# Optimization experiments

Hardware: AMD Instinct MI355X
Metric: run time of the kernel (lower is better)

Reference implementation:

```python
import jax, jax.numpy as jnp
import numpy as np

S, B, D, H = 2048, 2, 1024, 16
DK = D // H
SCALE = 1.0 / np.sqrt(DK)


def setup_inputs() -> dict:
    key = jax.random.key(0)
    ks = jax.random.split(key, 8)
    return {
        "query": jax.random.normal(ks[0], (S, B, D), dtype=jnp.float32),
        "key": jax.random.normal(ks[1], (S, B, D), dtype=jnp.float32),
        "value": jax.random.normal(ks[2], (S, B, D), dtype=jnp.float32),
        "mask": jax.random.randint(ks[3], (B, S, S), 0, 2, dtype=jnp.int32),
        "in_proj_weight": jax.random.normal(ks[4], (3 * D, D), dtype=jnp.float32) * 0.02,
        "in_proj_bias": jax.random.normal(ks[5], (3 * D,), dtype=jnp.float32) * 0.02,
        "out_proj_weight": jax.random.normal(ks[6], (D, D), dtype=jnp.float32) * 0.02,
        "out_proj_bias": jax.random.normal(ks[7], (D,), dtype=jnp.float32) * 0.02,
    }


def reference(query, key, value, mask, in_proj_weight, in_proj_bias,
              out_proj_weight, out_proj_bias):
    seq_len, batch, d_model = query.shape
    # split fused in-projection: order is query, key, value
    Wq, Wk, Wv = in_proj_weight[:D], in_proj_weight[D:2 * D], in_proj_weight[2 * D:]
    bq, bk, bv = in_proj_bias[:D], in_proj_bias[D:2 * D], in_proj_bias[2 * D:]
    # PrepareForMultiHeadAttention: x @ W^T + b, then split heads -> [s, b, h, d_k]
    q = (query @ Wq.T + bq).reshape(seq_len, batch, H, DK)
    k = (key @ Wk.T + bk).reshape(key.shape[0], batch, H, DK)
    v = (value @ Wv.T + bv).reshape(value.shape[0], batch, H, DK)
    # scores [i, j, b, h] in float32, scaled
    scores = jnp.einsum('ibhd,jbhd->ijbh', q, k).astype(jnp.float32) * SCALE
    # mask: [b, q, k] -> permute(1,2,0) -> [q, k, b] -> unsqueeze(-1)
    m = jnp.transpose(mask, (1, 2, 0))[..., None]
    scores = jnp.where(m == 1, jnp.float32(-1e9), scores)
    # softmax over key axis (dim=1)
    attn = jax.nn.softmax(scores, axis=1)
    # dropout p=0.0 -> identity
    x = jnp.einsum('ijbh,jbhd->ibhd', attn, v).reshape(seq_len, batch, -1)
    return x @ out_proj_weight.T + out_proj_bias
```

## Files before the change

kernel.cpp:

```cpp
#include <hip/hip_runtime.h>
#include <hip/hip_bf16.h>

typedef unsigned short u16;
typedef unsigned int   u32;
typedef unsigned long long u64;
typedef __bf16 bf16x8 __attribute__((ext_vector_type(8)));
typedef float  f32x4  __attribute__((ext_vector_type(4)));

#define S_LEN  2048
#define BATCH  2
#define DMODEL 1024
#define NHEADS 16
#define DKH    64
#define MWORDS (S_LEN/64)
#define ATT_SCALE 0.125f
#define C2EXP 0.18033688011112f

__device__ __forceinline__ u16 f2bf(float f){
  u32 x = __builtin_bit_cast(u32, f);
  x += 0x7fffu + ((x >> 16) & 1u);
  return (u16)(x >> 16);
}
__device__ __forceinline__ bf16x8 ld8(const u16* p){ return *(const bf16x8*)p; }

__device__ __forceinline__ void gload16(const u16* g, u16* l){
  __builtin_amdgcn_global_load_lds(
      (const __attribute__((address_space(1))) u32*)(u64)g,
      (__attribute__((address_space(3))) u32*)(u64)l,
      16, 0, 0);
}

__global__ __launch_bounds__(256) void cvt_kernel(
    const float* __restrict__ a0, const float* __restrict__ a1, const float* __restrict__ a2,
    const float* __restrict__ wi, const float* __restrict__ wo, const int* __restrict__ msk,
    u16* __restrict__ d0, u16* __restrict__ d1, u16* __restrict__ d2,
    u16* __restrict__ dwi, u16* __restrict__ dwo, u64* __restrict__ mbits)
{
  int tid = blockIdx.x*256 + threadIdx.x;
  int stride = gridDim.x*256;
  const int NX = S_LEN*BATCH*DMODEL/4;
  for (int i = tid; i < NX; i += stride){
    f32x4 x0 = ((const f32x4*)a0)[i];
    f32x4 x1 = ((const f32x4*)a1)[i];
    f32x4 x2 = ((const f32x4*)a2)[i];
    ((ushort4*)d0)[i] = make_ushort4(f2bf(x0[0]), f2bf(x0[1]), f2bf(x0[2]), f2bf(x0[3]));
    ((ushort4*)d1)[i] = make_ushort4(f2bf(x1[0]), f2bf(x1[1]), f2bf(x1[2]), f2bf(x1[3]));
    ((ushort4*)d2)[i] = make_ushort4(f2bf(x2[0]), f2bf(x2[1]), f2bf(x2[2]), f2bf(x2[3]));
  }
  const int NWI = 3*DMODEL*DMODEL/4;
  for (int i = tid; i < NWI; i += stride){
    f32x4 x = ((const f32x4*)wi)[i];
    ((ushort4*)dwi)[i] = make_ushort4(f2bf(x[0]), f2bf(x[1]), f2bf(x[2]), f2bf(x[3]));
  }
  const int NWO = DMODEL*DMODEL/4;
  for (int i = tid; i < NWO; i += stride){
    f32x4 x = ((const f32x4*)wo)[i];
    ((ushort4*)dwo)[i] = make_ushort4(f2bf(x[0]), f2bf(x[1]), f2bf(x[2]), f2bf(x[3]));
  }
  int gw   = tid >> 6;
  int lane = threadIdx.x & 63;
  int nwaves = stride >> 6;
  const int NW = BATCH*S_LEN*MWORDS;
  for (int w = gw; w < NW; w += nwaves){
    int v = msk[(size_t)w*64 + lane];
    u64 bits = __ballot(v != 0);
    if (lane == 0) mbits[w] = bits;
  }
}

__device__ __forceinline__ void gemm128_loop(
    const u16* __restrict__ A, const u16* __restrict__ W,
    u16* abuf, u16* bbuf, int tid, f32x4 acc[4][4])
{
  int lane = tid & 63, quad = lane >> 4, r = lane & 15;
  int wv = tid >> 6, wm = (wv & 1)*64, wn = (wv >> 1)*64;
  int c0 = tid, c1 = tid + 256;
  int r0 = c0 >> 2, g0 = ((c0 & 3) ^ (r0 & 3))*8;
  int r1 = c1 >> 2, g1 = ((c1 & 3) ^ (r1 & 3))*8;
  const u16* ga0 = A + (size_t)r0*DMODEL + g0;
  const u16* ga1 = A + (size_t)r1*DMODEL + g1;
  const u16* gb0 = W + (size_t)r0*DMODEL + g0;
  const u16* gb1 = W + (size_t)r1*DMODEL + g1;
  u16* la0 = abuf + c0*8;  u16* la1 = abuf + c1*8;
  u16* lb0 = bbuf + c0*8;  u16* lb1 = bbuf + c1*8;
  int sw = (quad ^ (r & 3))*8;

  for (int k0 = 0; k0 < DMODEL; k0 += 32){
    __syncthreads();
    gload16(ga0 + k0, la0);
    gload16(ga1 + k0, la1);
    gload16(gb0 + k0, lb0);
    gload16(gb1 + k0, lb1);
    __syncthreads();
    bf16x8 af[4], bfr[4];
    #pragma unroll
    for (int i = 0; i < 4; ++i) af[i]  = ld8(&abuf[(wm + i*16 + r)*32 + sw]);
    #pragma unroll
    for (int i = 0; i < 4; ++i) bfr[i] = ld8(&bbuf[(wn + i*16 + r)*32 + sw]);
    #pragma unroll
    for (int mi = 0; mi < 4; ++mi)
      #pragma unroll
      for (int ni = 0; ni < 4; ++ni)
        acc[mi][ni] = __builtin_amdgcn_mfma_f32_16x16x32_bf16(af[mi], bfr[ni], acc[mi][ni], 0,0,0);
  }
}

__global__ __launch_bounds__(256) void qkv_proj_kernel(
    const u16* __restrict__ xq, const u16* __restrict__ xk, const u16* __restrict__ xv,
    const u16* __restrict__ w, const float* __restrict__ bias,
    u16* __restrict__ q_ws, u16* __restrict__ k_ws, u16* __restrict__ vt_ws)
{
  __shared__ __align__(16) u16 abuf[128*32];
  __shared__ __align__(16) u16 bbuf[128*32];
  int tid = threadIdx.x;
  int lane = tid & 63, quad = lane >> 4, r = lane & 15;
  int wv = tid >> 6, wm = (wv & 1)*64, wn = (wv >> 1)*64;
  int m0 = blockIdx.x*128, n0 = blockIdx.y*128;
  int t = n0 >> 10;
  const u16* X = (t == 0) ? xq : (t == 1) ? xk : xv;

  f32x4 acc[4][4] = {};
  gemm128_loop(X + (size_t)m0*DMODEL, w + (size_t)n0*DMODEL, abuf, bbuf, tid, acc);

  int mbase = m0 + wm, nbase = n0 + wn;
  #pragma unroll
  for (int ni = 0; ni < 4; ++ni){
    int n  = nbase + ni*16 + r;
    float bv = bias[n];
    int nn = n & (DMODEL-1);
    int h = nn >> 6, dk = nn & 63;
    #pragma unroll
    for (int mi = 0; mi < 4; ++mi){
      #pragma unroll
      for (int reg = 0; reg < 4; ++reg){
        int m = mbase + mi*16 + quad*4 + reg;
        int s = m >> 1, b = m & 1;
        u16 hv = f2bf(acc[mi][ni][reg] + bv);
        size_t bh = (size_t)(b*NHEADS + h);
        if (t == 0)      q_ws [(bh*S_LEN + s)*DKH + dk] = hv;
        else if (t == 1) k_ws [(bh*S_LEN + s)*DKH + dk] = hv;
        else             vt_ws[(bh*DKH + dk)*S_LEN + s] = hv;
      }
    }
  }
}

__global__ __launch_bounds__(256) void attn_kernel(
    const u16* __restrict__ q_ws, const u16* __restrict__ k_ws, const u16* __restrict__ vt_ws,
    const u64* __restrict__ mbits, u16* __restrict__ x_ws)
{
  __shared__ __align__(16) u16 kperm[64*64];
  __shared__ __align__(16) u16 vperm[64*64];
  __shared__ __align__(16) u16 pbuf[4][16*72];
  int tid  = threadIdx.x;
  int wv   = tid >> 6;
  int lane = tid & 63;
  int quad = lane >> 4, r = lane & 15;
  int bh = blockIdx.y;
  int b  = bh >> 4, h = bh & 15;
  int i0 = (blockIdx.x*4 + wv) * 16;

  const u16* Q  = q_ws  + (size_t)bh*S_LEN*DKH;
  const u16* K  = k_ws  + (size_t)bh*S_LEN*DKH;
  const u16* Vt = vt_ws + (size_t)bh*DKH*S_LEN;
  const u64* MB = mbits + ((size_t)b*S_LEN + (i0 + r))*MWORDS;

  const u16* gk0 = K  + (size_t)(16*wv + r)*DKH + quad*8;
  const u16* gk1 = gk0 + 32;
  const u16* gv0 = Vt + (size_t)(16*wv + r)*S_LEN + quad*8;
  const u16* gv1 = gv0 + 32;
  u16* lk = kperm + (size_t)wv*128*8;
  u16* lv = vperm + (size_t)wv*128*8;

  const u16* qrow = Q + (size_t)(i0 + r)*DKH + quad*8;
  bf16x8 qf0 = ld8(qrow), qf1 = ld8(qrow + 32);

  float l_part = 0.f;
  f32x4 o[4] = {};
  f32x4 z = {0.f, 0.f, 0.f, 0.f};
  u16* pl = pbuf[wv];

  for (int j0 = 0; j0 < S_LEN; j0 += 64){
    u64 mb = MB[j0 >> 6];
    __syncthreads();
    gload16(gk0, lk);  gload16(gk1, lk + 512);
    gload16(gv0, lv);  gload16(gv1, lv + 512);
    gk0 += 64*DKH; gk1 += 64*DKH; gv0 += 64; gv1 += 64;
    __syncthreads();

    float p[16];
    #pragma unroll
    for (int c = 0; c < 4; ++c){
      bf16x8 ka = ld8(&kperm[(2*c + 0)*512 + lane*8]);
      bf16x8 kb = ld8(&kperm[(2*c + 1)*512 + lane*8]);
      f32x4 s = __builtin_amdgcn_mfma_f32_16x16x32_bf16(ka, qf0, z, 0,0,0);
      s       = __builtin_amdgcn_mfma_f32_16x16x32_bf16(kb, qf1, s, 0,0,0);
      u32 mc = (u32)(mb >> (16*c + 4*quad));
      p[c*4+0] = (mc & 1u) ? 0.f : __builtin_amdgcn_exp2f(s[0]*C2EXP);
      p[c*4+1] = (mc & 2u) ? 0.f : __builtin_amdgcn_exp2f(s[1]*C2EXP);
      p[c*4+2] = (mc & 4u) ? 0.f : __builtin_amdgcn_exp2f(s[2]*C2EXP);
      p[c*4+3] = (mc & 8u) ? 0.f : __builtin_amdgcn_exp2f(s[3]*C2EXP);
      l_part += p[c*4+0] + p[c*4+1] + p[c*4+2] + p[c*4+3];
    }
    #pragma unroll
    for (int c = 0; c < 4; ++c){
      u32 e0 = __builtin_bit_cast(u32, p[c*4+0]) + 0x8000u;
      u32 o0 = __builtin_bit_cast(u32, p[c*4+1]) + 0x8000u;
      u32 e1 = __builtin_bit_cast(u32, p[c*4+2]) + 0x8000u;
      u32 o1 = __builtin_bit_cast(u32, p[c*4+3]) + 0x8000u;
      uint2 pk;
      pk.x = __builtin_amdgcn_perm(o0, e0, 0x07060302u);
      pk.y = __builtin_amdgcn_perm(o1, e1, 0x07060302u);
      *(uint2*)&pl[r*72 + 16*c + quad*4] = pk;
    }
    asm volatile("s_waitcnt lgkmcnt(0)" ::: "memory");
    bf16x8 pf0 = ld8(&pl[r*72 + quad*8]);
    bf16x8 pf1 = ld8(&pl[r*72 + 32 + quad*8]);
    #pragma unroll
    for (int tt = 0; tt < 4; ++tt){
      bf16x8 va = ld8(&vperm[(2*tt + 0)*512 + lane*8]);
      bf16x8 vb = ld8(&vperm[(2*tt + 1)*512 + lane*8]);
      o[tt] = __builtin_amdgcn_mfma_f32_16x16x32_bf16(pf0, va, o[tt], 0,0,0);
      o[tt] = __builtin_amdgcn_mfma_f32_16x16x32_bf16(pf1, vb, o[tt], 0,0,0);
    }
  }

  l_part += __shfl_xor(l_part, 16, 64);
  l_part += __shfl_xor(l_part, 32, 64);
  float l0 = 1.f/__shfl(l_part, quad*4+0, 64);
  float l1 = 1.f/__shfl(l_part, quad*4+1, 64);
  float l2 = 1.f/__shfl(l_part, quad*4+2, 64);
  float l3 = 1.f/__shfl(l_part, quad*4+3, 64);
  #pragma unroll
  for (int tt = 0; tt < 4; ++tt){
    int col = h*DKH + tt*16 + r;
    x_ws[((size_t)(i0 + quad*4 + 0)*BATCH + b)*DMODEL + col] = f2bf(o[tt][0]*l0);
    x_ws[((size_t)(i0 + quad*4 + 1)*BATCH + b)*DMODEL + col] = f2bf(o[tt][1]*l1);
    x_ws[((size_t)(i0 + quad*4 + 2)*BATCH + b)*DMODEL + col] = f2bf(o[tt][2]*l2);
    x_ws[((size_t)(i0 + quad*4 + 3)*BATCH + b)*DMODEL + col] = f2bf(o[tt][3]*l3);
  }
}

__global__ __launch_bounds__(256) void out_proj_kernel(
    const u16* __restrict__ x, const u16* __restrict__ w, const float* __restrict__ bias,
    float* __restrict__ out)
{
  __shared__ __align__(16) u16 abuf[128*32];
  __shared__ __align__(16) u16 bbuf[128*32];
  int tid = threadIdx.x;
  int lane = tid & 63, quad = lane >> 4, r = lane & 15;
  int wv = tid >> 6, wm = (wv & 1)*64, wn = (wv >> 1)*64;
  int m0 = blockIdx.x*128, n0 = blockIdx.y*128;

  f32x4 acc[4][4] = {};
  gemm128_loop(x + (size_t)m0*DMODEL, w + (size_t)n0*DMODEL, abuf, bbuf, tid, acc);

  int mbase = m0 + wm, nbase = n0 + wn;
  #pragma unroll
  for (int ni = 0; ni < 4; ++ni){
    int n = nbase + ni*16 + r;
    float bv = bias[n];
    #pragma unroll
    for (int mi = 0; mi < 4; ++mi){
      #pragma unroll
      for (int reg = 0; reg < 4; ++reg){
        int m = mbase + mi*16 + quad*4 + reg;
        out[(size_t)m*DMODEL + n] = acc[mi][ni][reg] + bv;
      }
    }
  }
}

extern "C" void kernel_launch(void* const* d_in, const int* in_sizes, int n_in,
                              void* d_out, int out_size, void* d_ws, size_t ws_size,
                              hipStream_t stream) {
  (void)in_sizes; (void)n_in; (void)out_size; (void)ws_size;
  const float* query = (const float*)d_in[0];
  const float* key   = (const float*)d_in[1];
  const float* value = (const float*)d_in[2];
  const int*   mask  = (const int*)d_in[3];
  const float* w_in  = (const float*)d_in[4];
  const float* b_in  = (const float*)d_in[5];
  const float* w_out = (const float*)d_in[6];
  const float* b_out = (const float*)d_in[7];
  float* out = (float*)d_out;

  const size_t TSZ = (size_t)BATCH*NHEADS*S_LEN*DKH;
  const size_t XSZ = (size_t)S_LEN*BATCH*DMODEL;
  u16* q_ws  = (u16*)d_ws;
  u16* k_ws  = q_ws  + TSZ;
  u16* vt_ws = k_ws  + TSZ;
  u16* x_ws  = vt_ws + TSZ;
  u16* xq_bf = x_ws  + XSZ;
  u16* xk_bf = xq_bf + XSZ;
  u16* xv_bf = xk_bf + XSZ;
  u16* wi_bf = xv_bf + XSZ;
  u16* wo_bf = wi_bf + (size_t)3*DMODEL*DMODEL;
  u64* mb_ws = (u64*)(wo_bf + (size_t)DMODEL*DMODEL);

  cvt_kernel<<<1024, 256, 0, stream>>>(query, key, value, w_in, w_out, mask,
                                       xq_bf, xk_bf, xv_bf, wi_bf, wo_bf, mb_ws);
  qkv_proj_kernel<<<dim3(32, 24), 256, 0, stream>>>(xq_bf, xk_bf, xv_bf, wi_bf, b_in,
                                                    q_ws, k_ws, vt_ws);
  attn_kernel<<<dim3(32, 32), 256, 0, stream>>>(q_ws, k_ws, vt_ws, mb_ws, x_ws);
  out_proj_kernel<<<dim3(32, 8), 256, 0, stream>>>(x_ws, wo_bf, b_out, out);
}
```

Measured before the change: 289.3 us.

## Split attention over key dimension into three chunks with a combine kernel

The attention kernel now splits the key sequence into three chunks via a third grid dimension. Each chunk writes unnormalized bf16 partial outputs and row sums into reused workspace buffers, and a new combine kernel sums them, normalizes, and writes the head-interleaved output. The row-sum computation moves from scalar adds to an MFMA against a vector of ones. This triples the grid to improve occupancy and parallelism on the many-CU device. In exchange it adds an extra kernel launch, extra global traffic for the partials, and bf16 rounding of the partial outputs.

```diff
diff --git a/kernel.cpp b/kernel.cpp
--- a/kernel.cpp
+++ b/kernel.cpp
@@ -6,6 +6,7 @@
 typedef unsigned long long u64;
 typedef __bf16 bf16x8 __attribute__((ext_vector_type(8)));
 typedef float  f32x4  __attribute__((ext_vector_type(4)));
+typedef unsigned short u16x8 __attribute__((ext_vector_type(8)));
 
 #define S_LEN  2048
 #define BATCH  2
@@ -13,6 +14,8 @@
 #define NHEADS 16
 #define DKH    64
 #define MWORDS (S_LEN/64)
+#define NSPLIT 3
+#define NROWS  (32*2048)
 #define ATT_SCALE 0.125f
 #define C2EXP 0.18033688011112f
 
@@ -21,6 +24,7 @@
   x += 0x7fffu + ((x >> 16) & 1u);
   return (u16)(x >> 16);
 }
+__device__ __forceinline__ float bf2f(u16 u){ u32 x = ((u32)u) << 16; return __builtin_bit_cast(float, x); }
 __device__ __forceinline__ bf16x8 ld8(const u16* p){ return *(const bf16x8*)p; }
 
 __device__ __forceinline__ void gload16(const u16* g, u16* l){
@@ -147,7 +151,7 @@
 
 __global__ __launch_bounds__(256) void attn_kernel(
     const u16* __restrict__ q_ws, const u16* __restrict__ k_ws, const u16* __restrict__ vt_ws,
-    const u64* __restrict__ mbits, u16* __restrict__ x_ws)
+    const u64* __restrict__ mbits, u16* __restrict__ opart, float* __restrict__ l_ws)
 {
   __shared__ __align__(16) u16 kperm[64*64];
   __shared__ __align__(16) u16 vperm[64*64];
@@ -157,17 +161,20 @@
   int lane = tid & 63;
   int quad = lane >> 4, r = lane & 15;
   int bh = blockIdx.y;
-  int b  = bh >> 4, h = bh & 15;
+  int b  = bh >> 4;
   int i0 = (blockIdx.x*4 + wv) * 16;
+  int ksz = blockIdx.z;
+  int jstart = ksz*704;
+  int jcount = (ksz == 2) ? 10 : 11;
 
   const u16* Q  = q_ws  + (size_t)bh*S_LEN*DKH;
   const u16* K  = k_ws  + (size_t)bh*S_LEN*DKH;
   const u16* Vt = vt_ws + (size_t)bh*DKH*S_LEN;
   const u64* MB = mbits + ((size_t)b*S_LEN + (i0 + r))*MWORDS;
 
-  const u16* gk0 = K  + (size_t)(16*wv + r)*DKH + quad*8;
+  const u16* gk0 = K  + (size_t)(jstart + 16*wv + r)*DKH + quad*8;
   const u16* gk1 = gk0 + 32;
-  const u16* gv0 = Vt + (size_t)(16*wv + r)*S_LEN + quad*8;
+  const u16* gv0 = Vt + (size_t)(16*wv + r)*S_LEN + jstart + quad*8;
   const u16* gv1 = gv0 + 32;
   u16* lk = kperm + (size_t)wv*128*8;
   u16* lv = vperm + (size_t)wv*128*8;
@@ -175,12 +182,16 @@
   const u16* qrow = Q + (size_t)(i0 + r)*DKH + quad*8;
   bf16x8 qf0 = ld8(qrow), qf1 = ld8(qrow + 32);
 
-  float l_part = 0.f;
+  u16x8 onesu = {0x3F80,0x3F80,0x3F80,0x3F80,0x3F80,0x3F80,0x3F80,0x3F80};
+  bf16x8 ones1 = __builtin_bit_cast(bf16x8, onesu);
+
   f32x4 o[4] = {};
+  f32x4 l_acc = {0.f, 0.f, 0.f, 0.f};
   f32x4 z = {0.f, 0.f, 0.f, 0.f};
   u16* pl = pbuf[wv];
 
-  for (int j0 = 0; j0 < S_LEN; j0 += 64){
+  for (int it = 0; it < jcount; ++it){
+    int j0 = jstart + it*64;
     u64 mb = MB[j0 >> 6];
     __syncthreads();
     gload16(gk0, lk);  gload16(gk1, lk + 512);
@@ -200,7 +211,6 @@
       p[c*4+1] = (mc & 2u) ? 0.f : __builtin_amdgcn_exp2f(s[1]*C2EXP);
       p[c*4+2] = (mc & 4u) ? 0.f : __builtin_amdgcn_exp2f(s[2]*C2EXP);
       p[c*4+3] = (mc & 8u) ? 0.f : __builtin_amdgcn_exp2f(s[3]*C2EXP);
-      l_part += p[c*4+0] + p[c*4+1] + p[c*4+2] + p[c*4+3];
     }
     #pragma unroll
     for (int c = 0; c < 4; ++c){
@@ -216,6 +226,8 @@
     asm volatile("s_waitcnt lgkmcnt(0)" ::: "memory");
     bf16x8 pf0 = ld8(&pl[r*72 + quad*8]);
     bf16x8 pf1 = ld8(&pl[r*72 + 32 + quad*8]);
+    l_acc = __builtin_amdgcn_mfma_f32_16x16x32_bf16(pf0, ones1, l_acc, 0,0,0);
+    l_acc = __builtin_amdgcn_mfma_f32_16x16x32_bf16(pf1, ones1, l_acc, 0,0,0);
     #pragma unroll
     for (int tt = 0; tt < 4; ++tt){
       bf16x8 va = ld8(&vperm[(2*tt + 0)*512 + lane*8]);
@@ -225,19 +237,40 @@
     }
   }
 
-  l_part += __shfl_xor(l_part, 16, 64);
-  l_part += __shfl_xor(l_part, 32, 64);
-  float l0 = 1.f/__shfl(l_part, quad*4+0, 64);
-  float l1 = 1.f/__shfl(l_part, quad*4+1, 64);
-  float l2 = 1.f/__shfl(l_part, quad*4+2, 64);
-  float l3 = 1.f/__shfl(l_part, quad*4+3, 64);
+  size_t obase = (size_t)(ksz*32 + bh)*2048 + i0 + quad*4;
   #pragma unroll
   for (int tt = 0; tt < 4; ++tt){
-    int col = h*DKH + tt*16 + r;
-    x_ws[((size_t)(i0 + quad*4 + 0)*BATCH + b)*DMODEL + col] = f2bf(o[tt][0]*l0);
-    x_ws[((size_t)(i0 + quad*4 + 1)*BATCH + b)*DMODEL + col] = f2bf(o[tt][1]*l1);
-    x_ws[((size_t)(i0 + quad*4 + 2)*BATCH + b)*DMODEL + col] = f2bf(o[tt][2]*l2);
-    x_ws[((size_t)(i0 + quad*4 + 3)*BATCH + b)*DMODEL + col] = f2bf(o[tt][3]*l3);
+    #pragma unroll
+    for (int reg = 0; reg < 4; ++reg)
+      opart[(obase + reg)*64 + tt*16 + r] = f2bf(o[tt][reg]);
+  }
+  if (r == 0){
+    #pragma unroll
+    for (int reg = 0; reg < 4; ++reg) l_ws[obase + reg] = l_acc[reg];
+  }
+}
+
+__global__ __launch_bounds__(256) void combine_kernel(
+    const u16* __restrict__ opart, const float* __restrict__ l_ws, u16* __restrict__ x_ws)
+{
+  int row = blockIdx.x*256 + threadIdx.x;
+  int bh = row >> 11, i = row & 2047;
+  int b = bh >> 4, h = bh & 15;
+  float inv = 1.f/(l_ws[row] + l_ws[row + NROWS] + l_ws[row + 2*NROWS]);
+  const u16* p0 = opart + (size_t)row*64;
+  const u16* p1 = p0 + (size_t)NROWS*64;
+  const u16* p2 = p1 + (size_t)NROWS*64;
+  u16* xo = x_ws + ((size_t)i*BATCH + b)*DMODEL + h*64;
+  #pragma unroll
+  for (int c = 0; c < 8; ++c){
+    u16x8 a = *(const u16x8*)(p0 + c*8);
+    u16x8 bq = *(const u16x8*)(p1 + c*8);
+    u16x8 cq = *(const u16x8*)(p2 + c*8);
+    u16x8 rv;
+    #pragma unroll
+    for (int j = 0; j < 8; ++j)
+      rv[j] = f2bf((bf2f(a[j]) + bf2f(bq[j]) + bf2f(cq[j])) * inv);
+    *(u16x8*)(xo + c*8) = rv;
   }
 }
 
@@ -297,11 +330,15 @@
   u16* wi_bf = xv_bf + XSZ;
   u16* wo_bf = wi_bf + (size_t)3*DMODEL*DMODEL;
   u64* mb_ws = (u64*)(wo_bf + (size_t)DMODEL*DMODEL);
+  u16*   opart = xq_bf;
+  float* lpart = (float*)wi_bf;
 
   cvt_kernel<<<1024, 256, 0, stream>>>(query, key, value, w_in, w_out, mask,
                                        xq_bf, xk_bf, xv_bf, wi_bf, wo_bf, mb_ws);
   qkv_proj_kernel<<<dim3(32, 24), 256, 0, stream>>>(xq_bf, xk_bf, xv_bf, wi_bf, b_in,
                                                     q_ws, k_ws, vt_ws);
-  attn_kernel<<<dim3(32, 32), 256, 0, stream>>>(q_ws, k_ws, vt_ws, mb_ws, x_ws);
+  attn_kernel<<<dim3(32, 32, NSPLIT), 256, 0, stream>>>(q_ws, k_ws, vt_ws, mb_ws,
+                                                        opart, lpart);
+  combine_kernel<<<256, 256, 0, stream>>>(opart, lpart, x_ws);
   out_proj_kernel<<<dim3(32, 8), 256, 0, stream>>>(x_ws, wo_bf, b_out, out);
 }
```

Measured after the change: 308.7 us. 6.7% more time.
